# Kernel optimization log

Hardware: AMD Instinct MI355X
Metric: run time of the kernel (lower is better)

Reference implementation:

```python
import jax, jax.numpy as jnp
import numpy as np

PHI = (1.0 + 5.0 ** 0.5) / 2.0
TWO_PI = 2.0 * np.pi
LN_EPS = 1e-5


def _complex_linear(xr, xi, Wr, Wi, br, bi):
    # (Wr + i*Wi) @ (xr + i*xi) + (br + i*bi)
    yr = xr @ Wr.T - xi @ Wi.T + br
    yi = xr @ Wi.T + xi @ Wr.T + bi
    return yr, yi


def _layernorm(x, g, b):
    m = jnp.mean(x, axis=-1, keepdims=True)
    v = jnp.mean((x - m) ** 2, axis=-1, keepdims=True)
    return (x - m) * jax.lax.rsqrt(v + LN_EPS) * g + b


def reference(w, b, ip_Wr, ip_Wi, ip_br, ip_bi, ln_g, ln_b, W_qkv, log_alpha, op_Wr, op_Wi):
    B, S, D = w.shape
    H = log_alpha.shape[0]
    Dh = D // H
    scale = jnp.sqrt(jnp.asarray(Dh, w.dtype))
    alpha = jax.nn.sigmoid(log_alpha)[None, :, None]  # (1,H,1)
    ts = jnp.arange(S, dtype=w.dtype)

    def step(carry, xs):
        hr, hi, vs = carry          # (B,D),(B,D),(B,H,Dh)
        w_t, b_t, t = xs            # (B,D),(B,D),()
        # InstrumentedEulerTransform: separated theta, complex product
        wl = 1.0 + jnp.abs(w_t)
        tphi = (t * PHI) % TWO_PI   # wrap_time_periodic
        thr = hr / wl + b_t + tphi
        thi = hi / wl + b_t + tphi
        sr, cr = jnp.sin(thr), jnp.cos(thr)
        si, ci = jnp.sin(thi), jnp.cos(thi)
        hr2 = cr * ci - sr * si
        hi2 = cr * si + sr * ci
        # InstrumentedEchoChamber.forward_step
        pr, pi_ = _complex_linear(hr2, hi2, ip_Wr, ip_Wi, ip_br, ip_bi)
        xc = _layernorm(pr + pi_, ln_g, ln_b)
        qkv = (xc @ W_qkv.T).reshape(B, 3, H, Dh)
        q, k, v = qkv[:, 0], qkv[:, 1], qkv[:, 2]
        vs2 = alpha * v + (1.0 - alpha) * vs
        gate = jax.nn.sigmoid(jnp.sum(q * k, axis=-1, keepdims=True) / scale)
        retr = (gate * vs2).reshape(B, D)
        # output_proj ComplexLinear on (retr, 0), no bias
        ore = retr @ op_Wr.T
        oim = retr @ op_Wi.T
        return (hr2, hi2, vs2), (ore, oim)

    init = (jnp.zeros((B, D), w.dtype), jnp.zeros((B, D), w.dtype),
            jnp.zeros((B, H, Dh), w.dtype))
    wT = jnp.swapaxes(w, 0, 1)  # (S,B,D)
    bT = jnp.swapaxes(b, 0, 1)
    _, (or_seq, oi_seq) = jax.lax.scan(step, init, (wT, bT, ts))
    out = jnp.stack([or_seq, oi_seq])      # (2,S,B,D)
    return jnp.swapaxes(out, 1, 2)         # (2,B,S,D)


def setup_inputs() -> dict:
    key = jax.random.key(0)
    ks = jax.random.split(key, 10)
    B, S, D, H = 8, 2048, 512, 8
    s = 0.02
    return {
        "w": jax.random.normal(ks[0], (B, S, D), jnp.float32),
        "b": jax.random.normal(ks[1], (B, S, D), jnp.float32),
        "ip_Wr": jax.random.normal(ks[2], (D, D), jnp.float32) * s,
        "ip_Wi": jax.random.normal(ks[3], (D, D), jnp.float32) * s,
        "ip_br": jax.random.normal(ks[4], (D,), jnp.float32) * s,
        "ip_bi": jax.random.normal(ks[5], (D,), jnp.float32) * s,
        "ln_g": jnp.ones((D,), jnp.float32),
        "ln_b": jnp.zeros((D,), jnp.float32),
        "W_qkv": jax.random.normal(ks[6], (3 * D, D), jnp.float32) * s,
        "log_alpha": jax.random.normal(ks[7], (H,), jnp.float32),
        "op_Wr": jax.random.normal(ks[8], (D, D), jnp.float32) * s,
        "op_Wi": jax.random.normal(ks[9], (D, D), jnp.float32) * s,
    }
```

## Files before the change

kernel.cpp:

```cpp
#include <hip/hip_runtime.h>
#include <math.h>

#define BB 8
#define SS 2048
#define DD 512
#define HH 8
#define MM (BB*SS)

#define CHK 128
#define CL  16
#define CW  48

#define RT 32
#define RW 128

typedef unsigned short u16;
typedef unsigned int   u32;
typedef float f32x4 __attribute__((ext_vector_type(4)));
typedef short s16x8 __attribute__((ext_vector_type(8)));

__device__ __forceinline__ u16 f2bf(float x){
  union { float f; unsigned u; } c; c.f = x;
  unsigned r = c.u + 0x7FFF + ((c.u >> 16) & 1);
  return (u16)(r >> 16);
}
__device__ __forceinline__ float bf2f(u16 x){
  union { unsigned u; float f; } c; c.u = ((unsigned)x) << 16;
  return c.f;
}
__device__ __forceinline__ void gload16(const u16* g, u16* l){
  __builtin_amdgcn_global_load_lds(
      (const __attribute__((address_space(1))) unsigned int*)g,
      (__attribute__((address_space(3))) unsigned int*)l, 16, 0, 0);
}

__global__ void prep_all(const float* __restrict__ ipWr, const float* __restrict__ ipWi,
                         const float* __restrict__ Wqkv,
                         const float* __restrict__ opWr, const float* __restrict__ opWi,
                         const float* __restrict__ ipbr, const float* __restrict__ ipbi,
                         const float* __restrict__ la,
                         u16* __restrict__ W1, u16* __restrict__ Wq, u16* __restrict__ W3,
                         float* __restrict__ tphi2, float* __restrict__ bc,
                         float* __restrict__ alph){
  int id = blockIdx.x*256 + threadIdx.x;
  if (id < 524288){
    int n = id >> 10, k = id & 1023;
    int d = k >> 1;
    float v = (k & 1) ? (ipWr[n*512+d] - ipWi[n*512+d])
                      : (ipWr[n*512+d] + ipWi[n*512+d]);
    W1[id] = f2bf(v);
  } else if (id < 1310720){
    int i = id - 524288;
    Wq[i] = f2bf(Wqkv[i]);
  } else if (id < 1835008){
    int i = id - 1310720;
    int n = i >> 9, k = i & 511;
    W3[i] = f2bf((n < 512) ? opWr[n*512+k] : opWi[(n-512)*512+k]);
  } else if (id < 1837056){
    int t = id - 1835008;
    const float PHI_F    = 1.61803398874989484820f;
    const float TWO_PI_F = 6.28318530717958647693f;
    tphi2[t] = 2.0f * fmodf((float)t * PHI_F, TWO_PI_F);
  } else if (id < 1837568){
    int t = id - 1837056;
    bc[t] = ipbr[t] + ipbi[t];
  } else if (id < 1837576){
    int t = id - 1837568;
    alph[t] = 1.0f/(1.0f + expf(-la[t]));
  }
}

__global__ __launch_bounds__(256) void scan_h(const float* __restrict__ w,
                                              const float* __restrict__ bb,
                                              const float* __restrict__ tphi2,
                                              u32* __restrict__ X32){
  const int e = blockIdx.x*256 + threadIdx.x;
  const int c = blockIdx.y;
  const int b = e >> 9;
  const int d = e & 511;
  const float SQRT2 = 1.41421356237309504880f;
  const float PI_4  = 0.78539816339744830962f;
  const int tstart = c*CL;
  int t0 = tstart - CW; if (t0 < 0) t0 = 0;
  const int nw = tstart - t0;

  const float* wp = w  + ((size_t)b*SS + t0)*DD + d;
  const float* bp = bb + ((size_t)b*SS + t0)*DD + d;
  const float* tp = tphi2 + t0;

  const int U = 8;
  float wv[U], bv[U], wn[U], bn[U];

  float ss = 0.f;
  const int ngw = nw >> 3;
  if (ngw > 0){
    #pragma unroll
    for (int i=0;i<U;i++){ wv[i] = wp[(size_t)i*DD]; bv[i] = bp[(size_t)i*DD]; }
    for (int gg=0; gg<ngw; ++gg){
      if (gg+1 < ngw){
        const float* wnp = wp + (size_t)(gg+1)*U*DD;
        const float* bnp = bp + (size_t)(gg+1)*U*DD;
        #pragma unroll
        for (int i=0;i<U;i++){ wn[i] = wnp[(size_t)i*DD]; bn[i] = bnp[(size_t)i*DD]; }
      }
      #pragma unroll
      for (int i=0;i<U;i++){
        float rwl2 = SQRT2 * __builtin_amdgcn_rcpf(1.0f + fabsf(wv[i]));
        float cw   = fmaf(2.0f, bv[i], tp[gg*U+i]) + PI_4;
        ss = __sinf(fmaf(ss, rwl2, cw));
      }
      #pragma unroll
      for (int i=0;i<U;i++){ wv[i]=wn[i]; bv[i]=bn[i]; }
    }
  }
  float hs = SQRT2 * ss;

  const float* wq = wp + (size_t)nw*DD;
  const float* bq = bp + (size_t)nw*DD;
  const float* tq = tp + nw;
  u32* xp = X32 + (size_t)(b*SS + tstart)*512 + d;

  #pragma unroll
  for (int i=0;i<U;i++){ wv[i] = wq[(size_t)i*DD]; bv[i] = bq[(size_t)i*DD]; }
  for (int gg=0; gg<CL/U; ++gg){
    if (gg+1 < CL/U){
      const float* wnp = wq + (size_t)(gg+1)*U*DD;
      const float* bnp = bq + (size_t)(gg+1)*U*DD;
      #pragma unroll
      for (int i=0;i<U;i++){ wn[i] = wnp[(size_t)i*DD]; bn[i] = bnp[(size_t)i*DD]; }
    }
    #pragma unroll
    for (int i=0;i<U;i++){
      float rwl = __builtin_amdgcn_rcpf(1.0f + fabsf(wv[i]));
      float cc  = fmaf(2.0f, bv[i], tq[gg*U+i]);
      float theta = fmaf(hs, rwl, cc);
      float sn = __sinf(theta);
      float cs = __cosf(theta);
      hs = cs + sn;
      xp[(size_t)(gg*U+i)*512] = (u32)f2bf(cs) | ((u32)f2bf(sn) << 16);
    }
    #pragma unroll
    for (int i=0;i<U;i++){ wv[i]=wn[i]; bv[i]=bn[i]; }
  }
}

template<int TAG, int EPI>
__global__ __launch_bounds__(256) void gemm_bf16(const u16* __restrict__ A,
                                                 const u16* __restrict__ W,
                                                 float* __restrict__ C0,
                                                 float* __restrict__ C1,
                                                 u16* __restrict__ C2,
                                                 int N, int K){
  __shared__ __align__(16) u16 As[2][64*32];
  __shared__ __align__(16) u16 Bs[2][128*32];
  const int tid  = threadIdx.x;
  const int nwgx = gridDim.x;
  const int nwg  = nwgx * gridDim.y;
  const int lin  = blockIdx.y * nwgx + blockIdx.x;
  const int qq   = nwg >> 3;
  const int logi = (lin & 7) * qq + (lin >> 3);
  const int m0   = (logi / nwgx) * 64;
  const int n0   = (logi % nwgx) * 128;

  const int wave = tid >> 6;
  const int lane = tid & 63;
  const int wm   = wave >> 1;
  const int wn   = wave & 1;
  const int l15  = lane & 15;
  const int g    = lane >> 4;

  const int kgs  = (tid & 3) ^ ((tid >> 3) & 3);
  const u16* Asrc  = A + (size_t)(m0 + (tid>>2)) * K + kgs*8;
  const u16* Bsrc0 = W + (size_t)(n0 + (tid>>2)) * K + kgs*8;
  const u16* Bsrc1 = Bsrc0 + (size_t)64 * K;
  const int dA  = tid*8;
  const int dB0 = tid*8;
  const int dB1 = tid*8 + 2048;

  f32x4 acc[2][4];
  #pragma unroll
  for (int i=0;i<2;i++)
    #pragma unroll
    for (int j=0;j<4;j++) acc[i][j] = (f32x4){0.f,0.f,0.f,0.f};

#define STAGE(buf, koff) do {                 \
    gload16(Asrc  + (koff), &As[buf][dA]);    \
    gload16(Bsrc0 + (koff), &Bs[buf][dB0]);   \
    gload16(Bsrc1 + (koff), &Bs[buf][dB1]);   \
  } while(0)

#define COMPUTE(buf) do {                                            \
    s16x8 af[2], bf[4];                                              \
    _Pragma("unroll")                                                \
    for (int s=0;s<2;s++){                                           \
      int rA = wm*32 + s*16 + l15;                                   \
      af[s] = *(const s16x8*)&As[buf][rA*32 + ((g ^ ((rA>>1)&3))*8)];\
    }                                                                \
    _Pragma("unroll")                                                \
    for (int s=0;s<4;s++){                                           \
      int rB = wn*64 + s*16 + l15;                                   \
      bf[s] = *(const s16x8*)&Bs[buf][rB*32 + ((g ^ ((rB>>1)&3))*8)];\
    }                                                                \
    _Pragma("unroll")                                                \
    for (int mi=0;mi<2;mi++)                                         \
      _Pragma("unroll")                                              \
      for (int ni=0;ni<4;ni++)                                       \
        acc[mi][ni] = __builtin_amdgcn_mfma_f32_16x16x32_bf16(af[mi], bf[ni], acc[mi][ni], 0, 0, 0); \
  } while(0)

  const int nt = K >> 5;
  STAGE(0, 0);
  int cur = 0;
  for (int t = 0; t < nt; ++t){
    if (t+1 < nt){
      STAGE(cur^1, (t+1)*32);
      asm volatile("s_waitcnt vmcnt(3)" ::: "memory");
    } else {
      asm volatile("s_waitcnt vmcnt(0)" ::: "memory");
    }
    __builtin_amdgcn_s_barrier();
    COMPUTE(cur);
    asm volatile("" ::: "memory");
    __builtin_amdgcn_s_barrier();
    cur ^= 1;
  }

#undef STAGE
#undef COMPUTE

  #pragma unroll
  for (int mi=0;mi<2;mi++){
    #pragma unroll
    for (int j=0;j<4;j++){
      int r = m0 + wm*32 + mi*16 + g*4 + j;
      #pragma unroll
      for (int ni=0;ni<4;ni++){
        int col = n0 + wn*64 + ni*16 + l15;
        float v = acc[mi][ni][j];
        if (EPI == 1){
          if (col < 512) C0[(size_t)r*512 + col]       = v;
          else           C1[(size_t)r*512 + (col-512)] = v;
        } else {
          C2[(size_t)r*N + col] = f2bf(v);
        }
      }
    }
  }
}

__global__ __launch_bounds__(256) void ln_kernel(const u16* __restrict__ y,
                                                 const float* __restrict__ bc,
                                                 const float* __restrict__ g,
                                                 const float* __restrict__ bb,
                                                 u16* __restrict__ xc){
  const int row  = blockIdx.x*4 + (threadIdx.x >> 6);
  const int lane = threadIdx.x & 63;
  s16x8 v = *(const s16x8*)(y + (size_t)row*512 + lane*8);
  float4 c0 = ((const float4*)bc)[lane*2];
  float4 c1 = ((const float4*)bc)[lane*2+1];
  float f[8];
  f[0] = bf2f((u16)v[0]) + c0.x; f[1] = bf2f((u16)v[1]) + c0.y;
  f[2] = bf2f((u16)v[2]) + c0.z; f[3] = bf2f((u16)v[3]) + c0.w;
  f[4] = bf2f((u16)v[4]) + c1.x; f[5] = bf2f((u16)v[5]) + c1.y;
  f[6] = bf2f((u16)v[6]) + c1.z; f[7] = bf2f((u16)v[7]) + c1.w;
  float s = 0.f, s2 = 0.f;
  #pragma unroll
  for (int i=0;i<8;i++){ s += f[i]; s2 = fmaf(f[i], f[i], s2); }
  #pragma unroll
  for (int off=32; off>0; off>>=1){ s += __shfl_xor(s, off); s2 += __shfl_xor(s2, off); }
  float mean = s * (1.0f/512.0f);
  float var  = s2 * (1.0f/512.0f) - mean*mean;
  float rstd = rsqrtf(var + 1e-5f);
  float4 g0 = ((const float4*)g)[lane*2],  g1 = ((const float4*)g)[lane*2+1];
  float4 b0 = ((const float4*)bb)[lane*2], b1 = ((const float4*)bb)[lane*2+1];
  s16x8 o;
  o[0] = (short)f2bf((f[0]-mean)*rstd*g0.x + b0.x);
  o[1] = (short)f2bf((f[1]-mean)*rstd*g0.y + b0.y);
  o[2] = (short)f2bf((f[2]-mean)*rstd*g0.z + b0.z);
  o[3] = (short)f2bf((f[3]-mean)*rstd*g0.w + b0.w);
  o[4] = (short)f2bf((f[4]-mean)*rstd*g1.x + b1.x);
  o[5] = (short)f2bf((f[5]-mean)*rstd*g1.y + b1.y);
  o[6] = (short)f2bf((f[6]-mean)*rstd*g1.z + b1.z);
  o[7] = (short)f2bf((f[7]-mean)*rstd*g1.w + b1.w);
  *(s16x8*)(xc + (size_t)row*512 + lane*8) = o;
}

__global__ __launch_bounds__(256) void retr_fused(const u16* __restrict__ qkv,
                                                  const float* __restrict__ alph,
                                                  u16* __restrict__ retr){
  const int wid  = blockIdx.x*4 + (threadIdx.x >> 6);
  const int lane = threadIdx.x & 63;
  const int c = wid & 63;
  const int h = (wid >> 6) & 7;
  const int b = wid >> 9;
  const float a  = alph[h];
  const float om = 1.0f - a;
  const int d  = h*64 + lane;
  const int t0 = c*RT;
  int w0 = t0 - RW; if (w0 < 0) w0 = 0;
  const int nw = t0 - w0;

  const u16* vp = qkv + ((size_t)(b*SS + w0))*1536 + 1024 + d;
  float vs = 0.f;
  {
    const int U = 8;
    float vv[U], vn[U];
    const int ng = nw >> 3;
    if (ng > 0){
      #pragma unroll
      for (int i=0;i<U;i++) vv[i] = bf2f(vp[(size_t)i*1536]);
      for (int gg=0; gg<ng; ++gg){
        if (gg+1 < ng){
          const u16* vnp = vp + (size_t)(gg+1)*U*1536;
          #pragma unroll
          for (int i=0;i<U;i++) vn[i] = bf2f(vnp[(size_t)i*1536]);
        }
        #pragma unroll
        for (int i=0;i<U;i++) vs = fmaf(a, vv[i], om*vs);
        #pragma unroll
        for (int i=0;i<U;i++) vv[i] = vn[i];
      }
    }
  }
  const u16* qp = qkv + ((size_t)(b*SS + t0))*1536 + d;
  u16* op = retr + ((size_t)(b*SS + t0))*512 + d;
  #pragma unroll 4
  for (int i=0;i<RT;i++){
    float q  = bf2f(qp[(size_t)i*1536]);
    float kk = bf2f(qp[(size_t)i*1536 + 512]);
    float v  = bf2f(qp[(size_t)i*1536 + 1024]);
    vs = fmaf(a, v, om*vs);
    float p = q*kk;
    #pragma unroll
    for (int off=32; off>0; off>>=1) p += __shfl_xor(p, off);
    float gate = 1.0f/(1.0f + __expf(-p*0.125f));
    op[(size_t)i*512] = f2bf(gate * vs);
  }
}

extern "C" void kernel_launch(void* const* d_in, const int* in_sizes, int n_in,
                              void* d_out, int out_size, void* d_ws, size_t ws_size,
                              hipStream_t stream) {
  const float* w    = (const float*)d_in[0];
  const float* b    = (const float*)d_in[1];
  const float* ipWr = (const float*)d_in[2];
  const float* ipWi = (const float*)d_in[3];
  const float* ipbr = (const float*)d_in[4];
  const float* ipbi = (const float*)d_in[5];
  const float* lng  = (const float*)d_in[6];
  const float* lnb  = (const float*)d_in[7];
  const float* Wqkv = (const float*)d_in[8];
  const float* la   = (const float*)d_in[9];
  const float* opWr = (const float*)d_in[10];
  const float* opWi = (const float*)d_in[11];
  float* out0 = (float*)d_out;
  float* out1 = out0 + (size_t)MM*DD;

  char* base = (char*)d_ws;
  u16*   W1    = (u16*)  (base + 0);
  u16*   Wq    = (u16*)  (base + 1048576);
  u16*   W3    = (u16*)  (base + 2621440);
  float* bc    = (float*)(base + 3670016);
  float* alph  = (float*)(base + 3672064);
  float* tphi2 = (float*)(base + 3672128);
  u32*   X32   = (u32*)  (base + 3680384);
  u16*   y     = (u16*)  (base + 37234816);
  u16*   xc    = (u16*)  (base + 54012032);
  u16*   qkv   = (u16*)  (base + 70789248);
  u16*   retr  = (u16*)X32;

  prep_all<<<7179,256,0,stream>>>(ipWr, ipWi, Wqkv, opWr, opWi, ipbr, ipbi, la,
                                  W1, Wq, W3, tphi2, bc, alph);

  scan_h<<<dim3(16,CHK),256,0,stream>>>(w, b, tphi2, X32);

  gemm_bf16<1,2><<<dim3(4,256),256,0,stream>>>((const u16*)X32, W1, nullptr, nullptr, y, 512, 1024);
  ln_kernel<<<4096,256,0,stream>>>(y, bc, lng, lnb, xc);
  gemm_bf16<2,2><<<dim3(12,256),256,0,stream>>>(xc, Wq, nullptr, nullptr, qkv, 1536, 512);

  retr_fused<<<1024,256,0,stream>>>(qkv, alph, retr);

  gemm_bf16<3,1><<<dim3(8,256),256,0,stream>>>(retr, W3, out0, out1, nullptr, 1024, 512);
}
```

Before: 169.1 us.

## Enlarge GEMM tiles to 128x256 with 4-stage LDS pipeline and MFMA priority

The bf16 GEMM grows from 64x128 tiles on 4 waves to 128x256 tiles on 8 waves (512 threads), each wave now computing a 64x64 sub-tile. The LDS ring goes from double to quadruple buffering, keeping three global-to-LDS stages in flight. Fragments are read into registers before the next stage is issued, and the MFMA block runs under raised s_setprio. The aim is more data reuse per byte loaded and better hiding of load latency. In exchange, LDS use (96KB) and register pressure rise, and the grid has fewer workgroups, which may hurt occupancy and the tail across CUs.

```diff
diff --git a/kernel.cpp b/kernel.cpp
--- a/kernel.cpp
+++ b/kernel.cpp
@@ -145,94 +145,91 @@
 }
 
 template<int TAG, int EPI>
-__global__ __launch_bounds__(256) void gemm_bf16(const u16* __restrict__ A,
+__global__ __launch_bounds__(512) void gemm_bf16(const u16* __restrict__ A,
                                                  const u16* __restrict__ W,
                                                  float* __restrict__ C0,
                                                  float* __restrict__ C1,
                                                  u16* __restrict__ C2,
                                                  int N, int K){
-  __shared__ __align__(16) u16 As[2][64*32];
-  __shared__ __align__(16) u16 Bs[2][128*32];
+  __shared__ __align__(16) u16 As[4][128*32];
+  __shared__ __align__(16) u16 Bs[4][256*32];
   const int tid  = threadIdx.x;
   const int nwgx = gridDim.x;
   const int nwg  = nwgx * gridDim.y;
   const int lin  = blockIdx.y * nwgx + blockIdx.x;
   const int qq   = nwg >> 3;
   const int logi = (lin & 7) * qq + (lin >> 3);
-  const int m0   = (logi / nwgx) * 64;
-  const int n0   = (logi % nwgx) * 128;
+  const int m0   = (logi / nwgx) * 128;
+  const int n0   = (logi % nwgx) * 256;
 
   const int wave = tid >> 6;
   const int lane = tid & 63;
-  const int wm   = wave >> 1;
-  const int wn   = wave & 1;
+  const int wm   = wave >> 2;
+  const int wn   = wave & 3;
   const int l15  = lane & 15;
   const int g    = lane >> 4;
 
   const int kgs  = (tid & 3) ^ ((tid >> 3) & 3);
   const u16* Asrc  = A + (size_t)(m0 + (tid>>2)) * K + kgs*8;
   const u16* Bsrc0 = W + (size_t)(n0 + (tid>>2)) * K + kgs*8;
-  const u16* Bsrc1 = Bsrc0 + (size_t)64 * K;
+  const u16* Bsrc1 = Bsrc0 + (size_t)128 * K;
   const int dA  = tid*8;
   const int dB0 = tid*8;
-  const int dB1 = tid*8 + 2048;
-
-  f32x4 acc[2][4];
-  #pragma unroll
-  for (int i=0;i<2;i++)
+  const int dB1 = tid*8 + 4096;
+
+  f32x4 acc[4][4];
+  #pragma unroll
+  for (int i=0;i<4;i++)
     #pragma unroll
     for (int j=0;j<4;j++) acc[i][j] = (f32x4){0.f,0.f,0.f,0.f};
 
-#define STAGE(buf, koff) do {                 \
-    gload16(Asrc  + (koff), &As[buf][dA]);    \
-    gload16(Bsrc0 + (koff), &Bs[buf][dB0]);   \
-    gload16(Bsrc1 + (koff), &Bs[buf][dB1]);   \
+#define STAGE(reg, koff) do {                  \
+    gload16(Asrc  + (koff), &As[reg][dA]);     \
+    gload16(Bsrc0 + (koff), &Bs[reg][dB0]);    \
+    gload16(Bsrc1 + (koff), &Bs[reg][dB1]);    \
   } while(0)
 
-#define COMPUTE(buf) do {                                            \
-    s16x8 af[2], bf[4];                                              \
-    _Pragma("unroll")                                                \
-    for (int s=0;s<2;s++){                                           \
-      int rA = wm*32 + s*16 + l15;                                   \
-      af[s] = *(const s16x8*)&As[buf][rA*32 + ((g ^ ((rA>>1)&3))*8)];\
-    }                                                                \
-    _Pragma("unroll")                                                \
-    for (int s=0;s<4;s++){                                           \
-      int rB = wn*64 + s*16 + l15;                                   \
-      bf[s] = *(const s16x8*)&Bs[buf][rB*32 + ((g ^ ((rB>>1)&3))*8)];\
-    }                                                                \
-    _Pragma("unroll")                                                \
-    for (int mi=0;mi<2;mi++)                                         \
-      _Pragma("unroll")                                              \
-      for (int ni=0;ni<4;ni++)                                       \
-        acc[mi][ni] = __builtin_amdgcn_mfma_f32_16x16x32_bf16(af[mi], bf[ni], acc[mi][ni], 0, 0, 0); \
-  } while(0)
-
-  const int nt = K >> 5;
+  const int H = K >> 5;
   STAGE(0, 0);
-  int cur = 0;
-  for (int t = 0; t < nt; ++t){
-    if (t+1 < nt){
-      STAGE(cur^1, (t+1)*32);
-      asm volatile("s_waitcnt vmcnt(3)" ::: "memory");
-    } else {
-      asm volatile("s_waitcnt vmcnt(0)" ::: "memory");
-    }
+  STAGE(1, 32);
+  STAGE(2, 64);
+  asm volatile("s_waitcnt vmcnt(6)" ::: "memory");
+  __builtin_amdgcn_s_barrier();
+
+  for (int h = 0; h < H; ++h){
+    const u16* Ah = &As[h & 3][0];
+    const u16* Bh = &Bs[h & 3][0];
+    s16x8 af[4], bf[4];
+    #pragma unroll
+    for (int s=0;s<4;s++){
+      int rA = wm*64 + s*16 + l15;
+      af[s] = *(const s16x8*)&Ah[rA*32 + ((g ^ ((rA>>1)&3))*8)];
+      int rB = wn*64 + s*16 + l15;
+      bf[s] = *(const s16x8*)&Bh[rB*32 + ((g ^ ((rB>>1)&3))*8)];
+    }
+    if (h + 3 < H) STAGE((h+3) & 3, (h+3)*32);
     __builtin_amdgcn_s_barrier();
-    COMPUTE(cur);
-    asm volatile("" ::: "memory");
+    __builtin_amdgcn_s_setprio(1);
+    #pragma unroll
+    for (int mi=0;mi<4;mi++)
+      #pragma unroll
+      for (int ni=0;ni<4;ni++)
+        acc[mi][ni] = __builtin_amdgcn_mfma_f32_16x16x32_bf16(af[mi], bf[ni], acc[mi][ni], 0, 0, 0);
+    __builtin_amdgcn_s_setprio(0);
+    int rem = H - 1 - h;
+    if      (rem >= 3) asm volatile("s_waitcnt vmcnt(6)" ::: "memory");
+    else if (rem == 2) asm volatile("s_waitcnt vmcnt(3)" ::: "memory");
+    else if (rem == 1) asm volatile("s_waitcnt vmcnt(0)" ::: "memory");
     __builtin_amdgcn_s_barrier();
-    cur ^= 1;
   }
 
 #undef STAGE
-#undef COMPUTE
-
-  #pragma unroll
-  for (int mi=0;mi<2;mi++){
+
+  #pragma unroll
+  for (int mi=0;mi<4;mi++){
     #pragma unroll
     for (int j=0;j<4;j++){
-      int r = m0 + wm*32 + mi*16 + g*4 + j;
+      int r = m0 + wm*64 + mi*16 + g*4 + j;
       #pragma unroll
       for (int ni=0;ni<4;ni++){
         int col = n0 + wn*64 + ni*16 + l15;
@@ -374,11 +371,11 @@
 
   scan_h<<<dim3(16,CHK),256,0,stream>>>(w, b, tphi2, X32);
 
-  gemm_bf16<1,2><<<dim3(4,256),256,0,stream>>>((const u16*)X32, W1, nullptr, nullptr, y, 512, 1024);
+  gemm_bf16<1,2><<<dim3(2,128),512,0,stream>>>((const u16*)X32, W1, nullptr, nullptr, y, 512, 1024);
   ln_kernel<<<4096,256,0,stream>>>(y, bc, lng, lnb, xc);
-  gemm_bf16<2,2><<<dim3(12,256),256,0,stream>>>(xc, Wq, nullptr, nullptr, qkv, 1536, 512);
+  gemm_bf16<2,2><<<dim3(6,128),512,0,stream>>>(xc, Wq, nullptr, nullptr, qkv, 1536, 512);
 
   retr_fused<<<1024,256,0,stream>>>(qkv, alph, retr);
 
-  gemm_bf16<3,1><<<dim3(8,256),256,0,stream>>>(retr, W3, out0, out1, nullptr, 1024, 512);
-}
+  gemm_bf16<3,1><<<dim3(4,128),512,0,stream>>>(retr, W3, out0, out1, nullptr, 1024, 512);
+}
```

New measurement: 163.2 us. -3.5%, faster.
